# Kernel optimization log

Hardware: AMD Instinct MI355X
Metric: run time of the kernel (lower is better)

## Reference

```python
import jax, jax.numpy as jnp
import numpy as np

N = 20000; E = 320000; F_IN = 128; H = 4; D = 32; HD = 128; G = 8; C = 10


def _ln(x, g, b):
    mu = x.mean(-1, keepdims=True)
    v = ((x - mu) ** 2).mean(-1, keepdims=True)
    return (x - mu) / jnp.sqrt(v + 1e-5) * g + b


def _tconv(x, src, dst, attr, Wq, Wk, Wv, We, Ws, bq, bk, bv, be, bs):
    # PyG TransformerConv (concat=True, beta=False, root_weight=True), eval mode
    n = x.shape[0]
    q = (x @ Wq + bq).reshape(n, H, D)[dst]            # [E,H,D] gather at targets i
    k = (x @ Wk + bk).reshape(n, H, D)[src]            # [E,H,D] gather at sources j
    v = (x @ Wv + bv).reshape(n, H, D)[src]
    ef = (attr @ We + be).reshape(-1, H, D)            # edge features lifted to [E,H,D]
    k = k + ef
    v = v + ef
    logit = (q * k).sum(-1) / jnp.sqrt(jnp.float32(D))  # [E,H]
    m = jax.ops.segment_max(logit, dst, num_segments=n)
    m = jnp.where(jnp.isfinite(m), m, 0.0)
    ex = jnp.exp(logit - m[dst])
    s = jax.ops.segment_sum(ex, dst, num_segments=n)
    alpha = ex / (s[dst] + 1e-16)                      # segment softmax over incoming edges
    out = jax.ops.segment_sum(v * alpha[..., None], dst, num_segments=n).reshape(n, HD)
    out = out + x @ Ws + bs                            # skip / root weight
    return out, alpha


def setup_inputs() -> dict:
    key = jax.random.key(0)
    ks = jax.random.split(key, 50)
    inp = {}
    inp["x"] = jax.random.normal(ks[0], (N, F_IN), jnp.float32)
    inp["edge_index"] = jax.random.randint(ks[1], (2, E), 0, N)
    inp["attr"] = jax.random.normal(ks[2], (E, 1), jnp.float32)
    inp["batch"] = jnp.sort(jax.random.randint(ks[3], (N,), 0, G))
    i = 4
    for l, din in zip((1, 2, 3), (F_IN, HD, HD)):
        for nm, shp in (("Wq", (din, HD)), ("Wk", (din, HD)), ("Wv", (din, HD)), ("We", (1, HD)), ("Ws", (din, HD))):
            inp[f"{nm}{l}"] = jax.random.normal(ks[i], shp, jnp.float32) * 0.05
            i += 1
        for nm in ("bq", "bk", "bv", "be", "bs"):
            inp[f"{nm}{l}"] = jnp.zeros((HD,), jnp.float32)
    inp["ln1_g"] = jnp.ones((HD,), jnp.float32); inp["ln1_b"] = jnp.zeros((HD,), jnp.float32)
    inp["ln2_g"] = jnp.ones((HD,), jnp.float32); inp["ln2_b"] = jnp.zeros((HD,), jnp.float32)
    inp["fc1_w"] = jax.random.normal(ks[i], (HD, HD), jnp.float32) * 0.05; i += 1
    inp["fc1_b"] = jnp.zeros((HD,), jnp.float32)
    inp["cln_g"] = jnp.ones((HD,), jnp.float32); inp["cln_b"] = jnp.zeros((HD,), jnp.float32)
    inp["fc2_w"] = jax.random.normal(ks[i], (HD, C), jnp.float32) * 0.05
    inp["fc2_b"] = jnp.zeros((C,), jnp.float32)
    return inp


def reference(x, edge_index, attr, batch,
              Wq1, Wk1, Wv1, We1, Ws1, bq1, bk1, bv1, be1, bs1,
              Wq2, Wk2, Wv2, We2, Ws2, bq2, bk2, bv2, be2, bs2,
              Wq3, Wk3, Wv3, We3, Ws3, bq3, bk3, bv3, be3, bs3,
              ln1_g, ln1_b, ln2_g, ln2_b,
              fc1_w, fc1_b, cln_g, cln_b, fc2_w, fc2_b):
    src, dst = edge_index[0], edge_index[1]
    h, a1 = _tconv(x, src, dst, attr, Wq1, Wk1, Wv1, We1, Ws1, bq1, bk1, bv1, be1, bs1)
    h = jax.nn.relu(_ln(h, ln1_g, ln1_b))              # dropout is identity in eval
    h, a2 = _tconv(h, src, dst, attr, Wq2, Wk2, Wv2, We2, Ws2, bq2, bk2, bv2, be2, bs2)
    h = jax.nn.relu(_ln(h, ln2_g, ln2_b))
    z, a3 = _tconv(h, src, dst, attr, Wq3, Wk3, Wv3, We3, Ws3, bq3, bk3, bv3, be3, bs3)
    # global mean pool over graphs
    cnt = jax.ops.segment_sum(jnp.ones((N,), z.dtype), batch, num_segments=G)
    z_pool = jax.ops.segment_sum(z, batch, num_segments=G) / jnp.maximum(cnt, 1.0)[:, None]
    # classifier
    hcl = jax.nn.relu(_ln(z_pool @ fc1_w + fc1_b, cln_g, cln_b))
    probs = jax.nn.softmax(hcl @ fc2_w + fc2_b, axis=1)
    z_sel = z_pool[batch[0]]
    return (z, z_sel, probs, a1, a2, a3)
```

## Files before the change

kernel.cpp:

```cpp
#include <hip/hip_runtime.h>


typedef short short8v __attribute__((ext_vector_type(8)));
typedef float f32x4 __attribute__((ext_vector_type(4)));

__device__ __forceinline__ unsigned pack_bf16_rne(float a, float b) {
    unsigned ua = __float_as_uint(a);
    ua += 0x7fffu + ((ua >> 16) & 1u);
    unsigned ub = __float_as_uint(b);
    ub += 0x7fffu + ((ub >> 16) & 1u);
    return (ua >> 16) | (ub & 0xffff0000u);
}

__device__ __forceinline__ unsigned short bf16_rne1(float a) {
    unsigned u = __float_as_uint(a);
    u += 0x7fffu + ((u >> 16) & 1u);
    return (unsigned short)(u >> 16);
}

__device__ __forceinline__ float blo(unsigned u) { return __uint_as_float(u << 16); }
__device__ __forceinline__ float bhi(unsigned u) { return __uint_as_float(u & 0xffff0000u); }

__global__ __launch_bounds__(256) void hist_kernel(const int* __restrict__ dst,
                                                   int* __restrict__ cnt, int E) {
    int e = blockIdx.x * 256 + threadIdx.x;
    if (e < E) atomicAdd(&cnt[dst[e]], 1);
}

__global__ __launch_bounds__(256) void blk_reduce_kernel(const int* __restrict__ cnt,
                                                         int* __restrict__ bsum, int n) {
    __shared__ int ws[4];
    const int i = blockIdx.x * 256 + threadIdx.x;
    const int lane = threadIdx.x & 63, wid = threadIdx.x >> 6;
    int v = (i < n) ? cnt[i] : 0;
#pragma unroll
    for (int off = 1; off < 64; off <<= 1) v += __shfl_xor(v, off);
    if (lane == 0) ws[wid] = v;
    __syncthreads();
    if (threadIdx.x == 0) bsum[blockIdx.x] = ws[0] + ws[1] + ws[2] + ws[3];
}

__global__ __launch_bounds__(1024) void blk_scan_kernel(int* __restrict__ bsum, int nb) {
    __shared__ int wls[16];
    const int tid = threadIdx.x, lane = tid & 63, wid = tid >> 6;
    int v = (tid < nb) ? bsum[tid] : 0;
    int sc = v;
#pragma unroll
    for (int off = 1; off < 64; off <<= 1) {
        int t = __shfl_up(sc, off);
        if (lane >= off) sc += t;
    }
    if (lane == 63) wls[wid] = sc;
    __syncthreads();
    if (tid == 0) {
        int run = 0;
        for (int w = 0; w < 16; ++w) { int t = wls[w]; wls[w] = run; run += t; }
    }
    __syncthreads();
    if (tid < nb) bsum[tid] = wls[wid] + sc - v;
}

__global__ __launch_bounds__(256) void rowptr_fill_kernel(const int* __restrict__ cnt,
                                                          const int* __restrict__ boff,
                                                          int* __restrict__ rowptr, int n) {
    __shared__ int wls[4];
    const int i = blockIdx.x * 256 + threadIdx.x;
    const int lane = threadIdx.x & 63, wid = threadIdx.x >> 6;
    int v = (i < n) ? cnt[i] : 0;
    int sc = v;
#pragma unroll
    for (int off = 1; off < 64; off <<= 1) {
        int t = __shfl_up(sc, off);
        if (lane >= off) sc += t;
    }
    if (lane == 63) wls[wid] = sc;
    __syncthreads();
    int add = boff[blockIdx.x];
    for (int w = 0; w < wid; ++w) add += wls[w];
    if (i < n) rowptr[i + 1] = sc + add;
    if (i == 0) rowptr[0] = 0;
}

__global__ __launch_bounds__(256) void fill_kernel(const int* __restrict__ src,
                                                   const int* __restrict__ dst,
                                                   const float* __restrict__ attr,
                                                   const int* __restrict__ rowptr,
                                                   int* __restrict__ tmp,
                                                   int* __restrict__ src_perm,
                                                   float* __restrict__ attr_perm,
                                                   int* __restrict__ eidp, int E) {
    int e = blockIdx.x * 256 + threadIdx.x;
    if (e < E) {
        int d = dst[e];
        int p = atomicAdd(&tmp[d], 1);
        int pos = rowptr[d] + p;
        src_perm[pos] = src[e];
        attr_perm[pos] = attr[e];
        eidp[pos] = e;
    }
}

__global__ __launch_bounds__(256) void cvt_bf16_kernel(const float* __restrict__ in,
                                                       unsigned* __restrict__ outp, int n32) {
    int i = blockIdx.x * 256 + threadIdx.x;
    if (i < n32) {
        float2 v = *(const float2*)&in[(size_t)i * 2];
        outp[i] = pack_bf16_rne(v.x, v.y);
    }
}

struct W12 { const float* p[12]; };
__global__ __launch_bounds__(256) void prepack_all_kernel(W12 ws, unsigned* __restrict__ wt) {
    const int m = blockIdx.y;
    const float* W = ws.p[m];
    int idx = blockIdx.x * 256 + threadIdx.x;
    int c = idx >> 6;
    int kp = idx & 63;
    wt[(size_t)m * 8192 + (size_t)c * 64 + kp] =
        pack_bf16_rne(W[(size_t)(2 * kp) * 128 + c], W[(size_t)(2 * kp + 1) * 128 + c]);
}

__global__ __launch_bounds__(256) void gemm_mfma_kernel(
    const unsigned short* __restrict__ Xb, const unsigned short* __restrict__ wt,
    const float* __restrict__ bq, const float* __restrict__ bk,
    const float* __restrict__ bv, const float* __restrict__ bs,
    float* __restrict__ qo, unsigned short* __restrict__ ko,
    unsigned short* __restrict__ vo, float* __restrict__ so, int nrows) {
    const int lane = threadIdx.x & 63;
    const int w = threadIdx.x >> 6;
    const int m = blockIdx.y;
    const int strip = blockIdx.x * 64 + w * 16;
    const int arow = strip + (lane & 15);
    const int arow_c = min(arow, nrows - 1);
    const int kblk = (lane >> 4) * 8;
    const unsigned short* Wm = wt + (size_t)m * 16384;
    const float* bias = (m == 0) ? bq : (m == 1) ? bk : (m == 2) ? bv : bs;

    f32x4 acc[8];
#pragma unroll
    for (int f = 0; f < 8; ++f) acc[f] = (f32x4){0.f, 0.f, 0.f, 0.f};

#pragma unroll
    for (int ks = 0; ks < 4; ++ks) {
        const int k0 = ks * 32 + kblk;
        const short8v a = *(const short8v*)&Xb[(size_t)arow_c * 128 + k0];
#pragma unroll
        for (int f = 0; f < 8; ++f) {
            const short8v b = *(const short8v*)&Wm[(size_t)(f * 16 + (lane & 15)) * 128 + k0];
            acc[f] = __builtin_amdgcn_mfma_f32_16x16x32_bf16(a, b, acc[f], 0, 0, 0);
        }
    }

    const int r0 = strip + (lane >> 4) * 4;
#pragma unroll
    for (int f = 0; f < 8; ++f) {
        const int col = f * 16 + (lane & 15);
        const float bv_ = bias[col];
        if (m == 0 || m == 3) {
            float* OUT = (m == 0) ? qo : so;
#pragma unroll
            for (int r = 0; r < 4; ++r) {
                int row = r0 + r;
                if (row < nrows) OUT[(size_t)row * 128 + col] = acc[f][r] + bv_;
            }
        } else {
            unsigned short* OUT = (m == 1) ? ko : vo;
#pragma unroll
            for (int r = 0; r < 4; ++r) {
                int row = r0 + r;
                if (row < nrows) OUT[(size_t)row * 128 + col] = bf16_rne1(acc[f][r] + bv_);
            }
        }
    }
}

__global__ __launch_bounds__(256) void node_fused_kernel(
    const float* __restrict__ qb, const unsigned* __restrict__ kb,
    const unsigned* __restrict__ vb,
    const float* __restrict__ Wev, const float* __restrict__ bev,
    const int* __restrict__ rowptr, const int* __restrict__ src_perm,
    const float* __restrict__ attr_perm, const int* __restrict__ eidp,
    float* __restrict__ alpha_perm, float* __restrict__ alpha_out,
    const float* __restrict__ skip, float* __restrict__ zout,
    unsigned* __restrict__ hbout,
    const float* __restrict__ lng, const float* __restrict__ lnb,
    int do_ln, int n) {
    __shared__ float alds[4][64][4];
    const int wid = threadIdx.x >> 6;
    const int node = blockIdx.x * 4 + wid;
    const int lane = threadIdx.x & 63;
    if (node >= n) return;
    const int start = rowptr[node], end = rowptr[node + 1];
    const int deg = end - start;
    const int h = lane >> 4;
    const float we0 = Wev[2 * lane], we1 = Wev[2 * lane + 1];
    const float be0 = bev[2 * lane], be1 = bev[2 * lane + 1];
    const float2 qv = *(const float2*)&qb[(size_t)node * 128 + 2 * lane];
    const float scale = 0.17677669529663687f;
    const bool fastp = (deg <= 64);

    float acc0 = 0.f, acc1 = 0.f, sa = 0.f;

    if (deg > 0 && fastp) {
        float pw = qv.x * we0 + qv.y * we1;
        float pb = qv.x * be0 + qv.y * be1;
#pragma unroll
        for (int off = 1; off < 16; off <<= 1) {
            pw += __shfl_xor(pw, off);
            pb += __shfl_xor(pb, off);
        }

        const bool valid = lane < deg;
        const int j = start + lane;
        const int sj = valid ? src_perm[j] : 0;
        const float aj = valid ? attr_perm[j] : 0.f;

        int t = 0;
        for (; t + 3 < deg; t += 4) {
            const int s0 = __shfl(sj, t), s1 = __shfl(sj, t + 1);
            const int s2 = __shfl(sj, t + 2), s3 = __shfl(sj, t + 3);
            const float a0 = __shfl(aj, t), a1 = __shfl(aj, t + 1);
            const float a2 = __shfl(aj, t + 2), a3 = __shfl(aj, t + 3);
            const unsigned u0 = kb[(size_t)s0 * 64 + lane];
            const unsigned u1 = kb[(size_t)s1 * 64 + lane];
            const unsigned u2 = kb[(size_t)s2 * 64 + lane];
            const unsigned u3 = kb[(size_t)s3 * 64 + lane];
            float p0 = qv.x * blo(u0) + qv.y * bhi(u0);
            float p1 = qv.x * blo(u1) + qv.y * bhi(u1);
            float p2 = qv.x * blo(u2) + qv.y * bhi(u2);
            float p3 = qv.x * blo(u3) + qv.y * bhi(u3);
#pragma unroll
            for (int off = 1; off < 16; off <<= 1) {
                p0 += __shfl_xor(p0, off); p1 += __shfl_xor(p1, off);
                p2 += __shfl_xor(p2, off); p3 += __shfl_xor(p3, off);
            }
            if ((lane & 15) == 0) {
                alds[wid][t + 0][h] = (p0 + a0 * pw + pb) * scale;
                alds[wid][t + 1][h] = (p1 + a1 * pw + pb) * scale;
                alds[wid][t + 2][h] = (p2 + a2 * pw + pb) * scale;
                alds[wid][t + 3][h] = (p3 + a3 * pw + pb) * scale;
            }
        }
        for (; t < deg; ++t) {
            const int s0 = __shfl(sj, t);
            const float a0 = __shfl(aj, t);
            const unsigned u0 = kb[(size_t)s0 * 64 + lane];
            float p0 = qv.x * blo(u0) + qv.y * bhi(u0);
#pragma unroll
            for (int off = 1; off < 16; off <<= 1) p0 += __shfl_xor(p0, off);
            if ((lane & 15) == 0) alds[wid][t][h] = (p0 + a0 * pw + pb) * scale;
        }

        float4 lg = valid ? *(const float4*)&alds[wid][lane][0]
                          : make_float4(-1e30f, -1e30f, -1e30f, -1e30f);
        float4 mx = lg;
#pragma unroll
        for (int off = 1; off < 64; off <<= 1) {
            mx.x = fmaxf(mx.x, __shfl_xor(mx.x, off));
            mx.y = fmaxf(mx.y, __shfl_xor(mx.y, off));
            mx.z = fmaxf(mx.z, __shfl_xor(mx.z, off));
            mx.w = fmaxf(mx.w, __shfl_xor(mx.w, off));
        }
        float4 ev;
        ev.x = __expf(lg.x - mx.x); ev.y = __expf(lg.y - mx.y);
        ev.z = __expf(lg.z - mx.z); ev.w = __expf(lg.w - mx.w);
        float4 s4 = ev;
#pragma unroll
        for (int off = 1; off < 64; off <<= 1) {
            s4.x += __shfl_xor(s4.x, off); s4.y += __shfl_xor(s4.y, off);
            s4.z += __shfl_xor(s4.z, off); s4.w += __shfl_xor(s4.w, off);
        }
        float4 al;
        al.x = ev.x / (s4.x + 1e-16f); al.y = ev.y / (s4.y + 1e-16f);
        al.z = ev.z / (s4.z + 1e-16f); al.w = ev.w / (s4.w + 1e-16f);
        if (valid) *(float4*)&alpha_out[(size_t)eidp[j] * 4] = al;
        *(float4*)&alds[wid][lane][0] = al;

        t = 0;
        for (; t + 3 < deg; t += 4) {
            const int s0 = __shfl(sj, t), s1 = __shfl(sj, t + 1);
            const int s2 = __shfl(sj, t + 2), s3 = __shfl(sj, t + 3);
            const float a0 = __shfl(aj, t), a1 = __shfl(aj, t + 1);
            const float a2 = __shfl(aj, t + 2), a3 = __shfl(aj, t + 3);
            const float w0 = alds[wid][t + 0][h];
            const float w1 = alds[wid][t + 1][h];
            const float w2 = alds[wid][t + 2][h];
            const float w3 = alds[wid][t + 3][h];
            const unsigned u0 = vb[(size_t)s0 * 64 + lane];
            const unsigned u1 = vb[(size_t)s1 * 64 + lane];
            const unsigned u2 = vb[(size_t)s2 * 64 + lane];
            const unsigned u3 = vb[(size_t)s3 * 64 + lane];
            acc0 += w0 * blo(u0) + w1 * blo(u1) + w2 * blo(u2) + w3 * blo(u3);
            acc1 += w0 * bhi(u0) + w1 * bhi(u1) + w2 * bhi(u2) + w3 * bhi(u3);
            sa += w0 * a0 + w1 * a1 + w2 * a2 + w3 * a3;
        }
        for (; t < deg; ++t) {
            const int s0 = __shfl(sj, t);
            const float a0 = __shfl(aj, t);
            const float w0 = alds[wid][t][h];
            const unsigned u0 = vb[(size_t)s0 * 64 + lane];
            acc0 += w0 * blo(u0);
            acc1 += w0 * bhi(u0);
            sa += w0 * a0;
        }
    } else if (deg > 0) {
        float mh = -1e30f;
        for (int c0 = start; c0 < end; c0 += 64) {
            const int nc = min(64, end - c0);
            const int sj = (lane < nc) ? src_perm[c0 + lane] : 0;
            const float aj = (lane < nc) ? attr_perm[c0 + lane] : 0.f;
            int t = 0;
            for (; t + 1 < nc; t += 2) {
                const int s0 = __shfl(sj, t), s1 = __shfl(sj, t + 1);
                const float a0 = __shfl(aj, t), a1 = __shfl(aj, t + 1);
                const unsigned u0 = kb[(size_t)s0 * 64 + lane];
                const unsigned u1 = kb[(size_t)s1 * 64 + lane];
                float p0 = qv.x * (blo(u0) + a0 * we0 + be0) + qv.y * (bhi(u0) + a0 * we1 + be1);
                float p1 = qv.x * (blo(u1) + a1 * we0 + be0) + qv.y * (bhi(u1) + a1 * we1 + be1);
#pragma unroll
                for (int off = 1; off < 16; off <<= 1) {
                    p0 += __shfl_xor(p0, off);
                    p1 += __shfl_xor(p1, off);
                }
                p0 *= scale; p1 *= scale;
                mh = fmaxf(mh, fmaxf(p0, p1));
                if ((lane & 15) == 0) {
                    alpha_perm[(size_t)(c0 + t) * 4 + h] = p0;
                    alpha_perm[(size_t)(c0 + t + 1) * 4 + h] = p1;
                }
            }
            if (t < nc) {
                const int s0 = __shfl(sj, t);
                const float a0 = __shfl(aj, t);
                const unsigned u0 = kb[(size_t)s0 * 64 + lane];
                float p0 = qv.x * (blo(u0) + a0 * we0 + be0) + qv.y * (bhi(u0) + a0 * we1 + be1);
#pragma unroll
                for (int off = 1; off < 16; off <<= 1) p0 += __shfl_xor(p0, off);
                p0 *= scale;
                mh = fmaxf(mh, p0);
                if ((lane & 15) == 0) alpha_perm[(size_t)(c0 + t) * 4 + h] = p0;
            }
        }
        const float m0 = __shfl(mh, 0), m1 = __shfl(mh, 16);
        const float m2 = __shfl(mh, 32), m3 = __shfl(mh, 48);

        float4 s4 = make_float4(0.f, 0.f, 0.f, 0.f);
        for (int c0 = start; c0 < end; c0 += 64) {
            const int j = c0 + lane;
            if (j < end) {
                float4 lg = *(const float4*)&alpha_perm[(size_t)j * 4];
                lg.x = __expf(lg.x - m0); lg.y = __expf(lg.y - m1);
                lg.z = __expf(lg.z - m2); lg.w = __expf(lg.w - m3);
                *(float4*)&alpha_perm[(size_t)j * 4] = lg;
                s4.x += lg.x; s4.y += lg.y; s4.z += lg.z; s4.w += lg.w;
            }
        }
#pragma unroll
        for (int off = 1; off < 64; off <<= 1) {
            s4.x += __shfl_xor(s4.x, off); s4.y += __shfl_xor(s4.y, off);
            s4.z += __shfl_xor(s4.z, off); s4.w += __shfl_xor(s4.w, off);
        }
        const float i0 = 1.f / (s4.x + 1e-16f), i1 = 1.f / (s4.y + 1e-16f);
        const float i2 = 1.f / (s4.z + 1e-16f), i3 = 1.f / (s4.w + 1e-16f);

        for (int c0 = start; c0 < end; c0 += 64) {
            const int nc = min(64, end - c0);
            const int j = c0 + lane;
            if (lane < nc) {
                float4 ex = *(const float4*)&alpha_perm[(size_t)j * 4];
                float4 al;
                al.x = ex.x * i0; al.y = ex.y * i1; al.z = ex.z * i2; al.w = ex.w * i3;
                *(float4*)&alpha_out[(size_t)eidp[j] * 4] = al;
                *(float4*)&alds[wid][lane][0] = al;
            }
            const int sj = (lane < nc) ? src_perm[j] : 0;
            const float aj = (lane < nc) ? attr_perm[j] : 0.f;
            int t = 0;
            for (; t + 1 < nc; t += 2) {
                const int s0 = __shfl(sj, t), s1 = __shfl(sj, t + 1);
                const float a0 = __shfl(aj, t), a1 = __shfl(aj, t + 1);
                const float w0 = alds[wid][t][h];
                const float w1 = alds[wid][t + 1][h];
                const unsigned u0 = vb[(size_t)s0 * 64 + lane];
                const unsigned u1 = vb[(size_t)s1 * 64 + lane];
                acc0 += w0 * (blo(u0) + a0 * we0 + be0) + w1 * (blo(u1) + a1 * we0 + be0);
                acc1 += w0 * (bhi(u0) + a0 * we1 + be1) + w1 * (bhi(u1) + a1 * we1 + be1);
            }
            if (t < nc) {
                const int s0 = __shfl(sj, t);
                const float a0 = __shfl(aj, t);
                const float w0 = alds[wid][t][h];
                const unsigned u0 = vb[(size_t)s0 * 64 + lane];
                acc0 += w0 * (blo(u0) + a0 * we0 + be0);
                acc1 += w0 * (bhi(u0) + a0 * we1 + be1);
            }
        }
    }

    float2 o = *(const float2*)&skip[(size_t)node * 128 + 2 * lane];
    if (deg > 0) {
        if (fastp) {
            o.x += acc0 + sa * we0 + be0;
            o.y += acc1 + sa * we1 + be1;
        } else {
            o.x += acc0;
            o.y += acc1;
        }
    }
    if (do_ln) {
        float s = o.x + o.y;
#pragma unroll
        for (int off = 1; off < 64; off <<= 1) s += __shfl_xor(s, off);
        const float mu = s * (1.f / 128.f);
        const float d0 = o.x - mu, d1 = o.y - mu;
        float vs = d0 * d0 + d1 * d1;
#pragma unroll
        for (int off = 1; off < 64; off <<= 1) vs += __shfl_xor(vs, off);
        const float inv = rsqrtf(vs * (1.f / 128.f) + 1e-5f);
        const float2 gv = *(const float2*)&lng[2 * lane];
        const float2 bv2 = *(const float2*)&lnb[2 * lane];
        const float n0 = fmaxf(d0 * inv * gv.x + bv2.x, 0.f);
        const float n1 = fmaxf(d1 * inv * gv.y + bv2.y, 0.f);
        hbout[(size_t)node * 64 + lane] = pack_bf16_rne(n0, n1);
    } else {
        *(float2*)&zout[(size_t)node * 128 + 2 * lane] = o;
    }
}

__global__ __launch_bounds__(128) void pool_kernel(const float* __restrict__ z,
                                                   const int* __restrict__ batch,
                                                   float* __restrict__ pool,
                                                   int* __restrict__ gcnt, int n) {
    const int c = threadIdx.x;
    const int row0 = blockIdx.x * 32;
    if (row0 >= n) return;
    const int rend = min(row0 + 32, n);
    int cur = batch[row0];
    float acc = 0.f;
    int run = 0;
    for (int r = row0; r < rend; ++r) {
        const int g = batch[r];
        if (g != cur) {
            atomicAdd(&pool[cur * 128 + c], acc);
            if (c == 0) atomicAdd(&gcnt[cur], run);
            acc = 0.f; run = 0; cur = g;
        }
        acc += z[(size_t)r * 128 + c];
        ++run;
    }
    atomicAdd(&pool[cur * 128 + c], acc);
    if (c == 0) atomicAdd(&gcnt[cur], run);
}

__global__ __launch_bounds__(128) void classifier_kernel(
    const float* __restrict__ pool, const int* __restrict__ gcnt,
    const int* __restrict__ batch,
    const float* __restrict__ fc1_w, const float* __restrict__ fc1_b,
    const float* __restrict__ cg, const float* __restrict__ cbv,
    const float* __restrict__ fc2_w, const float* __restrict__ fc2_b,
    float* __restrict__ zsel, float* __restrict__ probs) {
    __shared__ float zp[8][128];
    __shared__ float hc[8][128];
    __shared__ float red[2];
    __shared__ float lgt[8][10];
    const int c = threadIdx.x;
    const int lane = c & 63, wid = c >> 6;
#pragma unroll
    for (int g = 0; g < 8; ++g)
        zp[g][c] = pool[g * 128 + c] / fmaxf((float)gcnt[g], 1.f);
    __syncthreads();
    zsel[c] = zp[batch[0]][c];

    float acc[8];
#pragma unroll
    for (int g = 0; g < 8; ++g) acc[g] = fc1_b[c];
    for (int k = 0; k < 128; ++k) {
        const float w = fc1_w[k * 128 + c];
#pragma unroll
        for (int g = 0; g < 8; ++g) acc[g] += zp[g][k] * w;
    }
#pragma unroll
    for (int g = 0; g < 8; ++g) {
        float s = acc[g];
        for (int off = 1; off < 64; off <<= 1) s += __shfl_xor(s, off);
        if (lane == 0) red[wid] = s;
        __syncthreads();
        const float mu = (red[0] + red[1]) * (1.f / 128.f);
        __syncthreads();
        const float d = acc[g] - mu;
        float s2 = d * d;
        for (int off = 1; off < 64; off <<= 1) s2 += __shfl_xor(s2, off);
        if (lane == 0) red[wid] = s2;
        __syncthreads();
        const float var = (red[0] + red[1]) * (1.f / 128.f);
        __syncthreads();
        hc[g][c] = fmaxf(d * rsqrtf(var + 1e-5f) * cg[c] + cbv[c], 0.f);
    }
    __syncthreads();
    if (c < 80) {
        const int g = c / 10, j = c - g * 10;
        float s = fc2_b[j];
        for (int k = 0; k < 128; ++k) s += hc[g][k] * fc2_w[k * 10 + j];
        lgt[g][j] = s;
    }
    __syncthreads();
    if (c < 8) {
        float mx = -1e30f;
#pragma unroll
        for (int j = 0; j < 10; ++j) mx = fmaxf(mx, lgt[c][j]);
        float ex[10];
        float sum = 0.f;
#pragma unroll
        for (int j = 0; j < 10; ++j) { ex[j] = expf(lgt[c][j] - mx); sum += ex[j]; }
#pragma unroll
        for (int j = 0; j < 10; ++j) probs[c * 10 + j] = ex[j] / sum;
    }
}


extern "C" void kernel_launch(void* const* d_in, const int* in_sizes, int n_in,
                              void* d_out, int out_size, void* d_ws, size_t ws_size,
                              hipStream_t stream) {
    const float* x = (const float*)d_in[0];
    const int* edge_index = (const int*)d_in[1];
    const float* attr = (const float*)d_in[2];
    const int* batch = (const int*)d_in[3];
    const int N = in_sizes[0] / 128;
    const int E = in_sizes[2];
    const int* src = edge_index;
    const int* dst = edge_index + E;

    const float *Wq[3], *Wk[3], *Wv[3], *We[3], *Ws[3];
    const float *bq[3], *bk[3], *bv[3], *be[3], *bs[3];
    int idx = 4;
    for (int l = 0; l < 3; ++l) {
        Wq[l] = (const float*)d_in[idx++];
        Wk[l] = (const float*)d_in[idx++];
        Wv[l] = (const float*)d_in[idx++];
        We[l] = (const float*)d_in[idx++];
        Ws[l] = (const float*)d_in[idx++];
        bq[l] = (const float*)d_in[idx++];
        bk[l] = (const float*)d_in[idx++];
        bv[l] = (const float*)d_in[idx++];
        be[l] = (const float*)d_in[idx++];
        bs[l] = (const float*)d_in[idx++];
    }
    const float* ln_g[2] = {(const float*)d_in[34], (const float*)d_in[36]};
    const float* ln_b[2] = {(const float*)d_in[35], (const float*)d_in[37]};
    const float* fc1_w = (const float*)d_in[38];
    const float* fc1_b = (const float*)d_in[39];
    const float* cln_g = (const float*)d_in[40];
    const float* cln_b = (const float*)d_in[41];
    const float* fc2_w = (const float*)d_in[42];
    const float* fc2_b = (const float*)d_in[43];
    const int C = in_sizes[43];

    float* out = (float*)d_out;
    float* z_out = out;
    float* zsel_out = out + (size_t)N * 128;
    float* probs_out = zsel_out + 128;
    const int GC = out_size - N * 128 - 128 - 3 * E * 4;
    const int G = GC / C;
    float* alpha_out[3];
    alpha_out[0] = probs_out + GC;
    alpha_out[1] = alpha_out[0] + (size_t)E * 4;
    alpha_out[2] = alpha_out[1] + (size_t)E * 4;

    char* p = (char*)d_ws;
    auto alloc = [&](size_t bytes) {
        void* r = (void*)p;
        p += (bytes + 255) & ~(size_t)255;
        return r;
    };
    float* qb = (float*)alloc((size_t)N * 128 * 4);
    unsigned* kb = (unsigned*)alloc((size_t)N * 64 * 4);
    unsigned* vb = (unsigned*)alloc((size_t)N * 64 * 4);
    float* hA = (float*)alloc((size_t)N * 128 * 4);
    unsigned* xb = (unsigned*)alloc((size_t)N * 64 * 4);
    unsigned* hb = (unsigned*)alloc((size_t)N * 64 * 4);
    unsigned* wt = (unsigned*)alloc((size_t)12 * 8192 * 4);
    int* counts = (int*)alloc((size_t)N * 4);
    int* rowptr = (int*)alloc((size_t)(N + 1) * 4);
    int* cnt2 = (int*)alloc((size_t)N * 4);
    int* bsum = (int*)alloc((size_t)1024 * 4);
    int* src_perm = (int*)alloc((size_t)E * 4);
    float* attr_perm = (float*)alloc((size_t)E * 4);
    int* eidp = (int*)alloc((size_t)E * 4);
    float* alpha_perm = (float*)alloc((size_t)E * 4 * 4);
    float* pool = (float*)alloc((size_t)G * 128 * 4);
    int* gcnt = (int*)alloc((size_t)G * 4);

    hipMemsetAsync(counts, 0, (size_t)N * 4, stream);
    hipMemsetAsync(cnt2, 0, (size_t)N * 4, stream);
    hipMemsetAsync(pool, 0, (size_t)G * 128 * 4, stream);
    hipMemsetAsync(gcnt, 0, (size_t)G * 4, stream);

    const int nb = (N + 255) / 256;
    hist_kernel<<<(E + 255) / 256, 256, 0, stream>>>(dst, counts, E);
    blk_reduce_kernel<<<nb, 256, 0, stream>>>(counts, bsum, N);
    blk_scan_kernel<<<1, 1024, 0, stream>>>(bsum, nb);
    rowptr_fill_kernel<<<nb, 256, 0, stream>>>(counts, bsum, rowptr, N);
    fill_kernel<<<(E + 255) / 256, 256, 0, stream>>>(src, dst, attr, rowptr, cnt2,
                                                     src_perm, attr_perm, eidp, E);

    cvt_bf16_kernel<<<(N * 64 + 255) / 256, 256, 0, stream>>>(x, xb, N * 64);
    W12 ws;
    for (int l = 0; l < 3; ++l) {
        ws.p[l * 4 + 0] = Wq[l]; ws.p[l * 4 + 1] = Wk[l];
        ws.p[l * 4 + 2] = Wv[l]; ws.p[l * 4 + 3] = Ws[l];
    }
    prepack_all_kernel<<<dim3(32, 12), 256, 0, stream>>>(ws, wt);

    for (int l = 0; l < 3; ++l) {
        float* SKIP = (l < 2) ? hA : z_out;
        const unsigned short* Xin = (const unsigned short*)((l == 0) ? xb : hb);
        gemm_mfma_kernel<<<dim3((N + 63) / 64, 4), 256, 0, stream>>>(
            Xin, (const unsigned short*)(wt + (size_t)l * 4 * 8192),
            bq[l], bk[l], bv[l], bs[l],
            qb, (unsigned short*)kb, (unsigned short*)vb, SKIP, N);
        node_fused_kernel<<<(N + 3) / 4, 256, 0, stream>>>(
            qb, kb, vb, We[l], be[l], rowptr, src_perm, attr_perm, eidp,
            alpha_perm, alpha_out[l], SKIP, z_out, hb,
            (l < 2) ? ln_g[l] : ln_g[0], (l < 2) ? ln_b[l] : ln_b[0],
            (l < 2) ? 1 : 0, N);
    }

    pool_kernel<<<(N + 31) / 32, 128, 0, stream>>>(z_out, batch, pool, gcnt, N);
    classifier_kernel<<<1, 128, 0, stream>>>(pool, gcnt, batch, fc1_w, fc1_b,
                                             cln_g, cln_b, fc2_w, fc2_b,
                                             zsel_out, probs_out);
}
```

Before: 501.8 us.

## Interleave K/V rows and fuse attention into single-pass online softmax

K and V are now stored interleaved per node in one buffer, so each source row's key and value are fetched together in a single gather pass. The fast path (degree ≤ 64) replaces the two-pass scheme (logits, then softmax, then a second V gather) with a streaming online softmax that rescales the accumulators per edge. Alpha is then recomputed from the stored logits using the final max and sum. The GEMM kernel now computes two weight matrices per block, halving grid.y and reusing the A fragment across Q/K and V/S. The cost is extra exp calls per edge for rescaling and more accumulator registers in the GEMM.

New measurement: 444.6 us. 11.4% less time.

```diff
diff --git a/kernel.cpp b/kernel.cpp
--- a/kernel.cpp
+++ b/kernel.cpp
@@ -124,21 +124,26 @@
     const unsigned short* __restrict__ Xb, const unsigned short* __restrict__ wt,
     const float* __restrict__ bq, const float* __restrict__ bk,
     const float* __restrict__ bv, const float* __restrict__ bs,
-    float* __restrict__ qo, unsigned short* __restrict__ ko,
-    unsigned short* __restrict__ vo, float* __restrict__ so, int nrows) {
+    float* __restrict__ qo, unsigned short* __restrict__ kvo,
+    float* __restrict__ so, int nrows) {
     const int lane = threadIdx.x & 63;
     const int w = threadIdx.x >> 6;
-    const int m = blockIdx.y;
+    const int pair = blockIdx.y;
     const int strip = blockIdx.x * 64 + w * 16;
     const int arow = strip + (lane & 15);
     const int arow_c = min(arow, nrows - 1);
     const int kblk = (lane >> 4) * 8;
-    const unsigned short* Wm = wt + (size_t)m * 16384;
-    const float* bias = (m == 0) ? bq : (m == 1) ? bk : (m == 2) ? bv : bs;
-
-    f32x4 acc[8];
-#pragma unroll
-    for (int f = 0; f < 8; ++f) acc[f] = (f32x4){0.f, 0.f, 0.f, 0.f};
+    const unsigned short* WmA = wt + (size_t)(pair * 2) * 16384;
+    const unsigned short* WmB = wt + (size_t)(pair * 2 + 1) * 16384;
+    const float* biasA = (pair == 0) ? bq : bv;
+    const float* biasB = (pair == 0) ? bk : bs;
+
+    f32x4 accA[8], accB[8];
+#pragma unroll
+    for (int f = 0; f < 8; ++f) {
+        accA[f] = (f32x4){0.f, 0.f, 0.f, 0.f};
+        accB[f] = (f32x4){0.f, 0.f, 0.f, 0.f};
+    }
 
 #pragma unroll
     for (int ks = 0; ks < 4; ++ks) {
@@ -146,8 +151,11 @@
         const short8v a = *(const short8v*)&Xb[(size_t)arow_c * 128 + k0];
 #pragma unroll
         for (int f = 0; f < 8; ++f) {
-            const short8v b = *(const short8v*)&Wm[(size_t)(f * 16 + (lane & 15)) * 128 + k0];
-            acc[f] = __builtin_amdgcn_mfma_f32_16x16x32_bf16(a, b, acc[f], 0, 0, 0);
+            const size_t boff = (size_t)(f * 16 + (lane & 15)) * 128 + k0;
+            const short8v b0 = *(const short8v*)&WmA[boff];
+            const short8v b1 = *(const short8v*)&WmB[boff];
+            accA[f] = __builtin_amdgcn_mfma_f32_16x16x32_bf16(a, b0, accA[f], 0, 0, 0);
+            accB[f] = __builtin_amdgcn_mfma_f32_16x16x32_bf16(a, b1, accB[f], 0, 0, 0);
         }
     }
 
@@ -155,28 +163,26 @@
 #pragma unroll
     for (int f = 0; f < 8; ++f) {
         const int col = f * 16 + (lane & 15);
-        const float bv_ = bias[col];
-        if (m == 0 || m == 3) {
-            float* OUT = (m == 0) ? qo : so;
-#pragma unroll
-            for (int r = 0; r < 4; ++r) {
-                int row = r0 + r;
-                if (row < nrows) OUT[(size_t)row * 128 + col] = acc[f][r] + bv_;
-            }
-        } else {
-            unsigned short* OUT = (m == 1) ? ko : vo;
-#pragma unroll
-            for (int r = 0; r < 4; ++r) {
-                int row = r0 + r;
-                if (row < nrows) OUT[(size_t)row * 128 + col] = bf16_rne1(acc[f][r] + bv_);
+        const float bA = biasA[col];
+        const float bB = biasB[col];
+#pragma unroll
+        for (int r = 0; r < 4; ++r) {
+            int row = r0 + r;
+            if (row < nrows) {
+                if (pair == 0) {
+                    qo[(size_t)row * 128 + col] = accA[f][r] + bA;
+                    kvo[(size_t)row * 256 + col] = bf16_rne1(accB[f][r] + bB);
+                } else {
+                    kvo[(size_t)row * 256 + 128 + col] = bf16_rne1(accA[f][r] + bA);
+                    so[(size_t)row * 128 + col] = accB[f][r] + bB;
+                }
             }
         }
     }
 }
 
 __global__ __launch_bounds__(256) void node_fused_kernel(
-    const float* __restrict__ qb, const unsigned* __restrict__ kb,
-    const unsigned* __restrict__ vb,
+    const float* __restrict__ qb, const unsigned* __restrict__ kv,
     const float* __restrict__ Wev, const float* __restrict__ bev,
     const int* __restrict__ rowptr, const int* __restrict__ src_perm,
     const float* __restrict__ attr_perm, const int* __restrict__ eidp,
@@ -209,11 +215,12 @@
             pw += __shfl_xor(pw, off);
             pb += __shfl_xor(pb, off);
         }
-
         const bool valid = lane < deg;
         const int j = start + lane;
         const int sj = valid ? src_perm[j] : 0;
         const float aj = valid ? attr_perm[j] : 0.f;
+
+        float m = -1e30f, s = 0.f;
 
         int t = 0;
         for (; t + 3 < deg; t += 4) {
@@ -221,100 +228,109 @@
             const int s2 = __shfl(sj, t + 2), s3 = __shfl(sj, t + 3);
             const float a0 = __shfl(aj, t), a1 = __shfl(aj, t + 1);
             const float a2 = __shfl(aj, t + 2), a3 = __shfl(aj, t + 3);
-            const unsigned u0 = kb[(size_t)s0 * 64 + lane];
-            const unsigned u1 = kb[(size_t)s1 * 64 + lane];
-            const unsigned u2 = kb[(size_t)s2 * 64 + lane];
-            const unsigned u3 = kb[(size_t)s3 * 64 + lane];
-            float p0 = qv.x * blo(u0) + qv.y * bhi(u0);
-            float p1 = qv.x * blo(u1) + qv.y * bhi(u1);
-            float p2 = qv.x * blo(u2) + qv.y * bhi(u2);
-            float p3 = qv.x * blo(u3) + qv.y * bhi(u3);
+            const unsigned uk0 = kv[(size_t)s0 * 128 + lane];
+            const unsigned uv0 = kv[(size_t)s0 * 128 + 64 + lane];
+            const unsigned uk1 = kv[(size_t)s1 * 128 + lane];
+            const unsigned uv1 = kv[(size_t)s1 * 128 + 64 + lane];
+            const unsigned uk2 = kv[(size_t)s2 * 128 + lane];
+            const unsigned uv2 = kv[(size_t)s2 * 128 + 64 + lane];
+            const unsigned uk3 = kv[(size_t)s3 * 128 + lane];
+            const unsigned uv3 = kv[(size_t)s3 * 128 + 64 + lane];
+            float p0 = qv.x * blo(uk0) + qv.y * bhi(uk0);
+            float p1 = qv.x * blo(uk1) + qv.y * bhi(uk1);
+            float p2 = qv.x * blo(uk2) + qv.y * bhi(uk2);
+            float p3 = qv.x * blo(uk3) + qv.y * bhi(uk3);
 #pragma unroll
             for (int off = 1; off < 16; off <<= 1) {
                 p0 += __shfl_xor(p0, off); p1 += __shfl_xor(p1, off);
                 p2 += __shfl_xor(p2, off); p3 += __shfl_xor(p3, off);
             }
+            p0 = (p0 + a0 * pw + pb) * scale;
+            p1 = (p1 + a1 * pw + pb) * scale;
+            p2 = (p2 + a2 * pw + pb) * scale;
+            p3 = (p3 + a3 * pw + pb) * scale;
             if ((lane & 15) == 0) {
-                alds[wid][t + 0][h] = (p0 + a0 * pw + pb) * scale;
-                alds[wid][t + 1][h] = (p1 + a1 * pw + pb) * scale;
-                alds[wid][t + 2][h] = (p2 + a2 * pw + pb) * scale;
-                alds[wid][t + 3][h] = (p3 + a3 * pw + pb) * scale;
+                alds[wid][t + 0][h] = p0;
+                alds[wid][t + 1][h] = p1;
+                alds[wid][t + 2][h] = p2;
+                alds[wid][t + 3][h] = p3;
+            }
+            {
+                const float mn = fmaxf(m, p0);
+                const float f = __expf(m - mn), w = __expf(p0 - mn);
+                acc0 = acc0 * f + w * blo(uv0);
+                acc1 = acc1 * f + w * bhi(uv0);
+                s = s * f + w; sa = sa * f + w * a0; m = mn;
+            }
+            {
+                const float mn = fmaxf(m, p1);
+                const float f = __expf(m - mn), w = __expf(p1 - mn);
+                acc0 = acc0 * f + w * blo(uv1);
+                acc1 = acc1 * f + w * bhi(uv1);
+                s = s * f + w; sa = sa * f + w * a1; m = mn;
+            }
+            {
+                const float mn = fmaxf(m, p2);
+                const float f = __expf(m - mn), w = __expf(p2 - mn);
+                acc0 = acc0 * f + w * blo(uv2);
+                acc1 = acc1 * f + w * bhi(uv2);
+                s = s * f + w; sa = sa * f + w * a2; m = mn;
+            }
+            {
+                const float mn = fmaxf(m, p3);
+                const float f = __expf(m - mn), w = __expf(p3 - mn);
+                acc0 = acc0 * f + w * blo(uv3);
+                acc1 = acc1 * f + w * bhi(uv3);
+                s = s * f + w; sa = sa * f + w * a3; m = mn;
             }
         }
         for (; t < deg; ++t) {
             const int s0 = __shfl(sj, t);
             const float a0 = __shfl(aj, t);
-            const unsigned u0 = kb[(size_t)s0 * 64 + lane];
-            float p0 = qv.x * blo(u0) + qv.y * bhi(u0);
+            const unsigned uk0 = kv[(size_t)s0 * 128 + lane];
+            const unsigned uv0 = kv[(size_t)s0 * 128 + 64 + lane];
+            float p0 = qv.x * blo(uk0) + qv.y * bhi(uk0);
 #pragma unroll
             for (int off = 1; off < 16; off <<= 1) p0 += __shfl_xor(p0, off);
-            if ((lane & 15) == 0) alds[wid][t][h] = (p0 + a0 * pw + pb) * scale;
-        }
-
-        float4 lg = valid ? *(const float4*)&alds[wid][lane][0]
-                          : make_float4(-1e30f, -1e30f, -1e30f, -1e30f);
-        float4 mx = lg;
-#pragma unroll
-        for (int off = 1; off < 64; off <<= 1) {
-            mx.x = fmaxf(mx.x, __shfl_xor(mx.x, off));
-            mx.y = fmaxf(mx.y, __shfl_xor(mx.y, off));
-            mx.z = fmaxf(mx.z, __shfl_xor(mx.z, off));
-            mx.w = fmaxf(mx.w, __shfl_xor(mx.w, off));
-        }
-        float4 ev;
-        ev.x = __expf(lg.x - mx.x); ev.y = __expf(lg.y - mx.y);
-        ev.z = __expf(lg.z - mx.z); ev.w = __expf(lg.w - mx.w);
-        float4 s4 = ev;
-#pragma unroll
-        for (int off = 1; off < 64; off <<= 1) {
-            s4.x += __shfl_xor(s4.x, off); s4.y += __shfl_xor(s4.y, off);
-            s4.z += __shfl_xor(s4.z, off); s4.w += __shfl_xor(s4.w, off);
-        }
-        float4 al;
-        al.x = ev.x / (s4.x + 1e-16f); al.y = ev.y / (s4.y + 1e-16f);
-        al.z = ev.z / (s4.z + 1e-16f); al.w = ev.w / (s4.w + 1e-16f);
-        if (valid) *(float4*)&alpha_out[(size_t)eidp[j] * 4] = al;
-        *(float4*)&alds[wid][lane][0] = al;
-
-        t = 0;
-        for (; t + 3 < deg; t += 4) {
-            const int s0 = __shfl(sj, t), s1 = __shfl(sj, t + 1);
-            const int s2 = __shfl(sj, t + 2), s3 = __shfl(sj, t + 3);
-            const float a0 = __shfl(aj, t), a1 = __shfl(aj, t + 1);
-            const float a2 = __shfl(aj, t + 2), a3 = __shfl(aj, t + 3);
-            const float w0 = alds[wid][t + 0][h];
-            const float w1 = alds[wid][t + 1][h];
-            const float w2 = alds[wid][t + 2][h];
-            const float w3 = alds[wid][t + 3][h];
-            const unsigned u0 = vb[(size_t)s0 * 64 + lane];
-            const unsigned u1 = vb[(size_t)s1 * 64 + lane];
-            const unsigned u2 = vb[(size_t)s2 * 64 + lane];
-            const unsigned u3 = vb[(size_t)s3 * 64 + lane];
-            acc0 += w0 * blo(u0) + w1 * blo(u1) + w2 * blo(u2) + w3 * blo(u3);
-            acc1 += w0 * bhi(u0) + w1 * bhi(u1) + w2 * bhi(u2) + w3 * bhi(u3);
-            sa += w0 * a0 + w1 * a1 + w2 * a2 + w3 * a3;
-        }
-        for (; t < deg; ++t) {
-            const int s0 = __shfl(sj, t);
-            const float a0 = __shfl(aj, t);
-            const float w0 = alds[wid][t][h];
-            const unsigned u0 = vb[(size_t)s0 * 64 + lane];
-            acc0 += w0 * blo(u0);
-            acc1 += w0 * bhi(u0);
-            sa += w0 * a0;
-        }
+            p0 = (p0 + a0 * pw + pb) * scale;
+            if ((lane & 15) == 0) alds[wid][t][h] = p0;
+            const float mn = fmaxf(m, p0);
+            const float f = __expf(m - mn), w = __expf(p0 - mn);
+            acc0 = acc0 * f + w * blo(uv0);
+            acc1 = acc1 * f + w * bhi(uv0);
+            s = s * f + w; sa = sa * f + w * a0; m = mn;
+        }
+
+        const float inv = 1.f / (s + 1e-16f);
+        acc0 *= inv; acc1 *= inv; sa *= inv;
+
+        const float m0 = __shfl(m, 0), m1 = __shfl(m, 16);
+        const float m2 = __shfl(m, 32), m3 = __shfl(m, 48);
+        const float i0 = __shfl(inv, 0), i1 = __shfl(inv, 16);
+        const float i2 = __shfl(inv, 32), i3 = __shfl(inv, 48);
+        if (valid) {
+            const float4 lg = *(const float4*)&alds[wid][lane][0];
+            float4 al;
+            al.x = __expf(lg.x - m0) * i0;
+            al.y = __expf(lg.y - m1) * i1;
+            al.z = __expf(lg.z - m2) * i2;
+            al.w = __expf(lg.w - m3) * i3;
+            *(float4*)&alpha_out[(size_t)eidp[j] * 4] = al;
+        }
+        acc0 += sa * we0;
+        acc1 += sa * we1;
     } else if (deg > 0) {
         float mh = -1e30f;
         for (int c0 = start; c0 < end; c0 += 64) {
             const int nc = min(64, end - c0);
-            const int sj = (lane < nc) ? src_perm[c0 + lane] : 0;
-            const float aj = (lane < nc) ? attr_perm[c0 + lane] : 0.f;
+            const int sjf = (lane < nc) ? src_perm[c0 + lane] : 0;
+            const float ajf = (lane < nc) ? attr_perm[c0 + lane] : 0.f;
             int t = 0;
             for (; t + 1 < nc; t += 2) {
-                const int s0 = __shfl(sj, t), s1 = __shfl(sj, t + 1);
-                const float a0 = __shfl(aj, t), a1 = __shfl(aj, t + 1);
-                const unsigned u0 = kb[(size_t)s0 * 64 + lane];
-                const unsigned u1 = kb[(size_t)s1 * 64 + lane];
+                const int s0 = __shfl(sjf, t), s1 = __shfl(sjf, t + 1);
+                const float a0 = __shfl(ajf, t), a1 = __shfl(ajf, t + 1);
+                const unsigned u0 = kv[(size_t)s0 * 128 + lane];
+                const unsigned u1 = kv[(size_t)s1 * 128 + lane];
                 float p0 = qv.x * (blo(u0) + a0 * we0 + be0) + qv.y * (bhi(u0) + a0 * we1 + be1);
                 float p1 = qv.x * (blo(u1) + a1 * we0 + be0) + qv.y * (bhi(u1) + a1 * we1 + be1);
 #pragma unroll
@@ -330,9 +346,9 @@
                 }
             }
             if (t < nc) {
-                const int s0 = __shfl(sj, t);
-                const float a0 = __shfl(aj, t);
-                const unsigned u0 = kb[(size_t)s0 * 64 + lane];
+                const int s0 = __shfl(sjf, t);
+                const float a0 = __shfl(ajf, t);
+                const unsigned u0 = kv[(size_t)s0 * 128 + lane];
                 float p0 = qv.x * (blo(u0) + a0 * we0 + be0) + qv.y * (bhi(u0) + a0 * we1 + be1);
 #pragma unroll
                 for (int off = 1; off < 16; off <<= 1) p0 += __shfl_xor(p0, off);
@@ -373,24 +389,24 @@
                 *(float4*)&alpha_out[(size_t)eidp[j] * 4] = al;
                 *(float4*)&alds[wid][lane][0] = al;
             }
-            const int sj = (lane < nc) ? src_perm[j] : 0;
-            const float aj = (lane < nc) ? attr_perm[j] : 0.f;
+            const int sjf = (lane < nc) ? src_perm[j] : 0;
+            const float ajf = (lane < nc) ? attr_perm[j] : 0.f;
             int t = 0;
             for (; t + 1 < nc; t += 2) {
-                const int s0 = __shfl(sj, t), s1 = __shfl(sj, t + 1);
-                const float a0 = __shfl(aj, t), a1 = __shfl(aj, t + 1);
+                const int s0 = __shfl(sjf, t), s1 = __shfl(sjf, t + 1);
+                const float a0 = __shfl(ajf, t), a1 = __shfl(ajf, t + 1);
                 const float w0 = alds[wid][t][h];
                 const float w1 = alds[wid][t + 1][h];
-                const unsigned u0 = vb[(size_t)s0 * 64 + lane];
-                const unsigned u1 = vb[(size_t)s1 * 64 + lane];
+                const unsigned u0 = kv[(size_t)s0 * 128 + 64 + lane];
+                const unsigned u1 = kv[(size_t)s1 * 128 + 64 + lane];
                 acc0 += w0 * (blo(u0) + a0 * we0 + be0) + w1 * (blo(u1) + a1 * we0 + be0);
                 acc1 += w0 * (bhi(u0) + a0 * we1 + be1) + w1 * (bhi(u1) + a1 * we1 + be1);
             }
             if (t < nc) {
-                const int s0 = __shfl(sj, t);
-                const float a0 = __shfl(aj, t);
+                const int s0 = __shfl(sjf, t);
+                const float a0 = __shfl(ajf, t);
                 const float w0 = alds[wid][t][h];
-                const unsigned u0 = vb[(size_t)s0 * 64 + lane];
+                const unsigned u0 = kv[(size_t)s0 * 128 + 64 + lane];
                 acc0 += w0 * (blo(u0) + a0 * we0 + be0);
                 acc1 += w0 * (bhi(u0) + a0 * we1 + be1);
             }
@@ -399,13 +415,8 @@
 
     float2 o = *(const float2*)&skip[(size_t)node * 128 + 2 * lane];
     if (deg > 0) {
-        if (fastp) {
-            o.x += acc0 + sa * we0 + be0;
-            o.y += acc1 + sa * we1 + be1;
-        } else {
-            o.x += acc0;
-            o.y += acc1;
-        }
+        o.x += acc0; o.y += acc1;
+        if (fastp) { o.x += be0; o.y += be1; }
     }
     if (do_ln) {
         float s = o.x + o.y;
@@ -573,8 +584,7 @@
         return r;
     };
     float* qb = (float*)alloc((size_t)N * 128 * 4);
-    unsigned* kb = (unsigned*)alloc((size_t)N * 64 * 4);
-    unsigned* vb = (unsigned*)alloc((size_t)N * 64 * 4);
+    unsigned* kv = (unsigned*)alloc((size_t)N * 128 * 4);
     float* hA = (float*)alloc((size_t)N * 128 * 4);
     unsigned* xb = (unsigned*)alloc((size_t)N * 64 * 4);
     unsigned* hb = (unsigned*)alloc((size_t)N * 64 * 4);
@@ -614,12 +624,12 @@
     for (int l = 0; l < 3; ++l) {
         float* SKIP = (l < 2) ? hA : z_out;
         const unsigned short* Xin = (const unsigned short*)((l == 0) ? xb : hb);
-        gemm_mfma_kernel<<<dim3((N + 63) / 64, 4), 256, 0, stream>>>(
+        gemm_mfma_kernel<<<dim3((N + 63) / 64, 2), 256, 0, stream>>>(
             Xin, (const unsigned short*)(wt + (size_t)l * 4 * 8192),
             bq[l], bk[l], bv[l], bs[l],
-            qb, (unsigned short*)kb, (unsigned short*)vb, SKIP, N);
+            qb, (unsigned short*)kv, SKIP, N);
         node_fused_kernel<<<(N + 3) / 4, 256, 0, stream>>>(
-            qb, kb, vb, We[l], be[l], rowptr, src_perm, attr_perm, eidp,
+            qb, kv, We[l], be[l], rowptr, src_perm, attr_perm, eidp,
             alpha_perm, alpha_out[l], SKIP, z_out, hb,
             (l < 2) ? ln_g[l] : ln_g[0], (l < 2) ? ln_b[l] : ln_b[0],
             (l < 2) ? 1 : 0, N);
```
